# Performance work log

Hardware: AMD Instinct MI355X
Metric: run time of the kernel (lower is better)

Reference implementation:

```python
import jax, jax.numpy as jnp
import numpy as np

D = 4096  # in_features == out_features (required: LayerNorm(in_features) applied to out-dim output)
B, S = 4, 4096
LN_EPS = 1e-5


def setup_inputs() -> dict:
    key = jax.random.key(0)
    ks = jax.random.split(key, 5)
    return {
        "x": jax.random.normal(ks[0], (B, S, D), dtype=jnp.float32),
        "weight": jax.random.normal(ks[1], (D, D), dtype=jnp.float32),  # [out, in]
        "bias": jax.random.normal(ks[2], (D,), dtype=jnp.float32),
        "g": jax.random.normal(ks[3], (D,), dtype=jnp.float32),   # input scale [in]
        "h": jax.random.normal(ks[4], (D,), dtype=jnp.float32),   # output scale [out]
        "ln_gamma": jnp.ones((D,), dtype=jnp.float32),
        "ln_beta": jnp.zeros((D,), dtype=jnp.float32),
    }


def reference(x, weight, bias, g, h, ln_gamma, ln_beta):
    sign_w = jnp.sign(weight)                      # binarized weight [out, in]
    xg = x * g                                     # per-input-channel scale
    y = jnp.einsum("bsi,oi->bso", xg, sign_w) + bias
    y = y * h                                      # per-output-channel scale
    mu = jnp.mean(y, axis=-1, keepdims=True)
    var = jnp.mean(jnp.square(y - mu), axis=-1, keepdims=True)
    out = (y - mu) * jax.lax.rsqrt(var + LN_EPS) * ln_gamma + ln_beta
    return out
```

## Files before the change

### kernel.cpp

```cpp
#include <hip/hip_runtime.h>
#include <hip/hip_bf16.h>
#include <stdint.h>

typedef __bf16 bf16x8 __attribute__((ext_vector_type(8)));
typedef float f32x4 __attribute__((ext_vector_type(4)));

#define GLDS16(gp, lp) __builtin_amdgcn_global_load_lds( \
    (const __attribute__((address_space(1))) unsigned int*)(gp), \
    (__attribute__((address_space(3))) unsigned int*)(lp), 16, 0, 0)

#define BARRIER() asm volatile("s_barrier" ::: "memory")
#define VMCNT(n)  asm volatile("s_waitcnt vmcnt(" #n ")" ::: "memory")


__global__ __launch_bounds__(256) void prep_xg(
    const float* __restrict__ x, const float* __restrict__ g,
    __bf16* __restrict__ out, long total, int K)
{
    long i = ((long)blockIdx.x * blockDim.x + threadIdx.x) * 8;
    const long stride = (long)gridDim.x * blockDim.x * 8;
    for (; i < total; i += stride) {
        const int k = (int)(i & (long)(K - 1));
        f32x4 x0 = *(const f32x4*)(x + i);
        f32x4 x1 = *(const f32x4*)(x + i + 4);
        f32x4 g0 = *(const f32x4*)(g + k);
        f32x4 g1 = *(const f32x4*)(g + k + 4);
        bf16x8 o;
        #pragma unroll
        for (int j = 0; j < 4; ++j) o[j]     = (__bf16)(x0[j] * g0[j]);
        #pragma unroll
        for (int j = 0; j < 4; ++j) o[4 + j] = (__bf16)(x1[j] * g1[j]);
        *(bf16x8*)(out + i) = o;
    }
}

__global__ __launch_bounds__(256) void prep_sign(
    const float* __restrict__ w, __bf16* __restrict__ out, long total)
{
    long i = ((long)blockIdx.x * blockDim.x + threadIdx.x) * 8;
    const long stride = (long)gridDim.x * blockDim.x * 8;
    for (; i < total; i += stride) {
        f32x4 w0 = *(const f32x4*)(w + i);
        f32x4 w1 = *(const f32x4*)(w + i + 4);
        bf16x8 o;
        #pragma unroll
        for (int j = 0; j < 4; ++j)
            o[j]     = (__bf16)((w0[j] > 0.f) ? 1.f : ((w0[j] < 0.f) ? -1.f : 0.f));
        #pragma unroll
        for (int j = 0; j < 4; ++j)
            o[4 + j] = (__bf16)((w1[j] > 0.f) ? 1.f : ((w1[j] < 0.f) ? -1.f : 0.f));
        *(bf16x8*)(out + i) = o;
    }
}


__global__ __launch_bounds__(512, 2) void gemm_8p(
    const __bf16* __restrict__ A, const __bf16* __restrict__ B,
    const float* __restrict__ bias, const float* __restrict__ h,
    float* __restrict__ y, int M, int N, int K)
{
    extern __shared__ __bf16 sm[];

    const int xcd = blockIdx.x & 7;
    const int l = blockIdx.x >> 3;
    const int bn = xcd * 2 + (l >> 6);
    const int bm = l & 63;

    const int t = threadIdx.x;
    const int lane = t & 63;
    const int w = t >> 6;
    const int wm = w >> 2;
    const int wn = w & 3;
    const int sl = lane >> 4;
    const int fr = lane & 15;

    const int ra8 = (wm * 16 + fr) * 8;
    const int rb8 = (wn * 16 + fr) * 8;
    const int stA = w * 2048 + lane * 8;
    const int stB = 16384 + stA;

    const __bf16* gA = A + (long)(bm * 256 + lane) * K + w * 8;
    const __bf16* gB = B + (long)(bn * 256 + lane) * K + w * 8;

    const int NT = K / 64;
    const long K64 = (long)K * 64;
    const long K128 = (long)K * 128;

#define STG_A(c, T, half) do { \
    GLDS16(gA + (long)(half) * K128 + (long)(T) * 64,             &sm[(c) * 32768 + stA + (half) * 1024]); \
    GLDS16(gA + (long)(half) * K128 + K64 + (long)(T) * 64,       &sm[(c) * 32768 + stA + (half) * 1024 + 512]); \
} while (0)
#define STG_B(c, T, half) do { \
    GLDS16(gB + (long)(half) * K128 + (long)(T) * 64,             &sm[(c) * 32768 + stB + (half) * 1024]); \
    GLDS16(gB + (long)(half) * K128 + K64 + (long)(T) * 64,       &sm[(c) * 32768 + stB + (half) * 1024 + 512]); \
} while (0)

#define RD_A(dst, cb, m, kk)  dst = *(bf16x8*)&sm[(cb) + ((kk) * 4 + sl) * 2048 + (m) * 256 + ra8]
#define RD_B(dst, cb, n, kk)  dst = *(bf16x8*)&sm[(cb) + 16384 + ((kk) * 4 + sl) * 2048 + (n) * 512 + rb8]
#define MF(d, a, b) d = __builtin_amdgcn_mfma_f32_16x16x32_bf16(a, b, d, 0, 0, 0)

    f32x4 acc[8][4] = {};
    bf16x8 aF[4][2], aH[4][2], b0F[2][2], b1F[2][2];

    STG_A(0, 0, 0); STG_B(0, 0, 0); STG_B(0, 0, 1); STG_A(0, 0, 1);
    STG_A(1, 1, 0); STG_B(1, 1, 0); STG_B(1, 1, 1);
    VMCNT(6);
    BARRIER();

    for (int i = 0; i < NT / 2; ++i) {
        const int t1 = 2 * i + 1;
        const int nx0 = 2 * i + 2;
        const int nx1 = 2 * i + 3;
        const bool more = (nx0 < NT);

        #pragma unroll
        for (int kk = 0; kk < 2; ++kk) {
            #pragma unroll
            for (int m = 0; m < 4; ++m) RD_A(aF[m][kk], 0, m, kk);
            #pragma unroll
            for (int n = 0; n < 2; ++n) RD_B(b0F[n][kk], 0, n, kk);
        }
        STG_A(1, t1, 1);
        BARRIER();
        __builtin_amdgcn_s_setprio(1);
        #pragma unroll
        for (int kk = 0; kk < 2; ++kk)
            #pragma unroll
            for (int m = 0; m < 4; ++m)
                #pragma unroll
                for (int n = 0; n < 2; ++n) MF(acc[m][n], aF[m][kk], b0F[n][kk]);
        __builtin_amdgcn_s_setprio(0);
        BARRIER();

        #pragma unroll
        for (int kk = 0; kk < 2; ++kk)
            #pragma unroll
            for (int n = 0; n < 2; ++n) RD_B(b1F[n][kk], 0, n + 2, kk);
        if (more) STG_A(0, nx0, 0);
        BARRIER();
        __builtin_amdgcn_s_setprio(1);
        #pragma unroll
        for (int kk = 0; kk < 2; ++kk)
            #pragma unroll
            for (int m = 0; m < 4; ++m)
                #pragma unroll
                for (int n = 0; n < 2; ++n) MF(acc[m][n + 2], aF[m][kk], b1F[n][kk]);
        __builtin_amdgcn_s_setprio(0);
        BARRIER();

        #pragma unroll
        for (int kk = 0; kk < 2; ++kk)
            #pragma unroll
            for (int m = 0; m < 4; ++m) RD_A(aH[m][kk], 0, m + 4, kk);
        if (more) STG_B(0, nx0, 0);
        BARRIER();
        __builtin_amdgcn_s_setprio(1);
        #pragma unroll
        for (int kk = 0; kk < 2; ++kk)
            #pragma unroll
            for (int m = 0; m < 4; ++m)
                #pragma unroll
                for (int n = 0; n < 2; ++n) MF(acc[m + 4][n], aH[m][kk], b0F[n][kk]);
        __builtin_amdgcn_s_setprio(0);
        BARRIER();

        if (more) { STG_B(0, nx0, 1); VMCNT(6); } else { VMCNT(0); }
        BARRIER();
        __builtin_amdgcn_s_setprio(1);
        #pragma unroll
        for (int kk = 0; kk < 2; ++kk)
            #pragma unroll
            for (int m = 0; m < 4; ++m)
                #pragma unroll
                for (int n = 0; n < 2; ++n) MF(acc[m + 4][n + 2], aH[m][kk], b1F[n][kk]);
        __builtin_amdgcn_s_setprio(0);
        BARRIER();

        #pragma unroll
        for (int kk = 0; kk < 2; ++kk) {
            #pragma unroll
            for (int m = 0; m < 4; ++m) RD_A(aF[m][kk], 32768, m, kk);
            #pragma unroll
            for (int n = 0; n < 2; ++n) RD_B(b0F[n][kk], 32768, n, kk);
        }
        if (more) STG_A(0, nx0, 1);
        BARRIER();
        __builtin_amdgcn_s_setprio(1);
        #pragma unroll
        for (int kk = 0; kk < 2; ++kk)
            #pragma unroll
            for (int m = 0; m < 4; ++m)
                #pragma unroll
                for (int n = 0; n < 2; ++n) MF(acc[m][n], aF[m][kk], b0F[n][kk]);
        __builtin_amdgcn_s_setprio(0);
        BARRIER();

        #pragma unroll
        for (int kk = 0; kk < 2; ++kk)
            #pragma unroll
            for (int n = 0; n < 2; ++n) RD_B(b1F[n][kk], 32768, n + 2, kk);
        if (more) STG_A(1, nx1, 0);
        BARRIER();
        __builtin_amdgcn_s_setprio(1);
        #pragma unroll
        for (int kk = 0; kk < 2; ++kk)
            #pragma unroll
            for (int m = 0; m < 4; ++m)
                #pragma unroll
                for (int n = 0; n < 2; ++n) MF(acc[m][n + 2], aF[m][kk], b1F[n][kk]);
        __builtin_amdgcn_s_setprio(0);
        BARRIER();

        #pragma unroll
        for (int kk = 0; kk < 2; ++kk)
            #pragma unroll
            for (int m = 0; m < 4; ++m) RD_A(aH[m][kk], 32768, m + 4, kk);
        if (more) STG_B(1, nx1, 0);
        BARRIER();
        __builtin_amdgcn_s_setprio(1);
        #pragma unroll
        for (int kk = 0; kk < 2; ++kk)
            #pragma unroll
            for (int m = 0; m < 4; ++m)
                #pragma unroll
                for (int n = 0; n < 2; ++n) MF(acc[m + 4][n], aH[m][kk], b0F[n][kk]);
        __builtin_amdgcn_s_setprio(0);
        BARRIER();

        if (more) { STG_B(1, nx1, 1); VMCNT(6); } else { VMCNT(0); }
        BARRIER();
        __builtin_amdgcn_s_setprio(1);
        #pragma unroll
        for (int kk = 0; kk < 2; ++kk)
            #pragma unroll
            for (int m = 0; m < 4; ++m)
                #pragma unroll
                for (int n = 0; n < 2; ++n) MF(acc[m + 4][n + 2], aH[m][kk], b1F[n][kk]);
        __builtin_amdgcn_s_setprio(0);
        BARRIER();
    }

    const int cr = (lane >> 4) * 4;
    const int cc = lane & 15;
    #pragma unroll
    for (int n = 0; n < 4; ++n) {
        const int col = bn * 256 + n * 64 + wn * 16 + cc;
        const float bc = bias[col];
        const float hc = h[col];
        #pragma unroll
        for (int m = 0; m < 8; ++m) {
            const long rowb = (long)bm * 256 + m * 32 + wm * 16 + cr;
            #pragma unroll
            for (int j = 0; j < 4; ++j)
                y[(rowb + j) * N + col] = (acc[m][n][j] + bc) * hc;
        }
    }
#undef STG_A
#undef STG_B
#undef RD_A
#undef RD_B
#undef MF
}


__global__ __launch_bounds__(256) void ln_inplace(
    float* __restrict__ y, const float* __restrict__ gamma,
    const float* __restrict__ beta, int N)
{
    const long row = blockIdx.x;
    float* p = y + row * (long)N;
    const int t = threadIdx.x;

    f32x4 v[4];
    float sum = 0.f, sq = 0.f;
    #pragma unroll
    for (int i = 0; i < 4; ++i) {
        v[i] = *(const f32x4*)(p + i * 1024 + t * 4);
        #pragma unroll
        for (int j = 0; j < 4; ++j) { sum += v[i][j]; sq += v[i][j] * v[i][j]; }
    }
    #pragma unroll
    for (int off = 32; off > 0; off >>= 1) {
        sum += __shfl_down(sum, off);
        sq  += __shfl_down(sq, off);
    }
    __shared__ float s1[4], s2[4];
    const int lane = t & 63, wave = t >> 6;
    if (lane == 0) { s1[wave] = sum; s2[wave] = sq; }
    __syncthreads();
    const float tot = s1[0] + s1[1] + s1[2] + s1[3];
    const float tsq = s2[0] + s2[1] + s2[2] + s2[3];
    const float mean = tot / (float)N;
    const float var = tsq / (float)N - mean * mean;
    const float rstd = rsqrtf(var + 1e-5f);

    #pragma unroll
    for (int i = 0; i < 4; ++i) {
        f32x4 ga = *(const f32x4*)(gamma + i * 1024 + t * 4);
        f32x4 be = *(const f32x4*)(beta + i * 1024 + t * 4);
        f32x4 o;
        #pragma unroll
        for (int j = 0; j < 4; ++j) o[j] = (v[i][j] - mean) * rstd * ga[j] + be[j];
        *(f32x4*)(p + i * 1024 + t * 4) = o;
    }
}


#define BMf 128
#define BNf 128
#define BKf 32
#define LDPf 40

__global__ __launch_bounds__(256) void binlin_gemm_fb(
    const float* __restrict__ x, const float* __restrict__ w,
    const float* __restrict__ bias, const float* __restrict__ g,
    const float* __restrict__ h, float* __restrict__ y,
    int M, int N, int K)
{
    __shared__ __bf16 As[BMf][LDPf];
    __shared__ __bf16 Bs[BNf][LDPf];
    const int nbn = N / BNf;
    const int bm = blockIdx.x / nbn;
    const int bn = blockIdx.x % nbn;
    const int t = threadIdx.x;
    const int lane = t & 63;
    const int wave = t >> 6;
    const int wm = wave >> 1, wn = wave & 1;
    const int row2 = t >> 2, kq = (t & 3) * 8;
    const long xbase = (long)bm * BMf * K;
    const long wbase = (long)bn * BNf * K;
    f32x4 acc[4][4] = {};
    const int fr = lane & 15;
    const int ko = (lane >> 4) * 8;
    for (int k0 = 0; k0 < K; k0 += BKf) {
        f32x4 ga = *(const f32x4*)(g + k0 + kq);
        f32x4 gb = *(const f32x4*)(g + k0 + kq + 4);
        #pragma unroll
        for (int p = 0; p < 2; ++p) {
            const int r = p * 64 + row2;
            const float* xp = x + xbase + (long)r * K + k0 + kq;
            f32x4 x0 = *(const f32x4*)xp;
            f32x4 x1 = *(const f32x4*)(xp + 4);
            bf16x8 av;
            #pragma unroll
            for (int i = 0; i < 4; ++i) av[i]     = (__bf16)(x0[i] * ga[i]);
            #pragma unroll
            for (int i = 0; i < 4; ++i) av[4 + i] = (__bf16)(x1[i] * gb[i]);
            *(bf16x8*)&As[r][kq] = av;
            const float* wp = w + wbase + (long)r * K + k0 + kq;
            f32x4 w0 = *(const f32x4*)wp;
            f32x4 w1 = *(const f32x4*)(wp + 4);
            bf16x8 bv;
            #pragma unroll
            for (int i = 0; i < 4; ++i)
                bv[i]     = (__bf16)((w0[i] > 0.f) ? 1.f : ((w0[i] < 0.f) ? -1.f : 0.f));
            #pragma unroll
            for (int i = 0; i < 4; ++i)
                bv[4 + i] = (__bf16)((w1[i] > 0.f) ? 1.f : ((w1[i] < 0.f) ? -1.f : 0.f));
            *(bf16x8*)&Bs[r][kq] = bv;
        }
        __syncthreads();
        bf16x8 af[4], bfr[4];
        #pragma unroll
        for (int m = 0; m < 4; ++m) af[m]  = *(bf16x8*)&As[wm * 64 + m * 16 + fr][ko];
        #pragma unroll
        for (int n = 0; n < 4; ++n) bfr[n] = *(bf16x8*)&Bs[wn * 64 + n * 16 + fr][ko];
        #pragma unroll
        for (int m = 0; m < 4; ++m)
            #pragma unroll
            for (int n = 0; n < 4; ++n)
                acc[m][n] = __builtin_amdgcn_mfma_f32_16x16x32_bf16(af[m], bfr[n], acc[m][n], 0, 0, 0);
        __syncthreads();
    }
    const int cr = (lane >> 4) * 4;
    const int cc = lane & 15;
    #pragma unroll
    for (int n = 0; n < 4; ++n) {
        const int col = bn * BNf + wn * 64 + n * 16 + cc;
        const float bc = bias[col];
        const float hc = h[col];
        #pragma unroll
        for (int m = 0; m < 4; ++m) {
            const long rowb = (long)bm * BMf + wm * 64 + m * 16 + cr;
            #pragma unroll
            for (int j = 0; j < 4; ++j)
                y[(rowb + j) * N + col] = (acc[m][n][j] + bc) * hc;
        }
    }
}

extern "C" void kernel_launch(void* const* d_in, const int* in_sizes, int n_in,
                              void* d_out, int out_size, void* d_ws, size_t ws_size,
                              hipStream_t stream)
{
    (void)n_in; (void)out_size;
    const float* x     = (const float*)d_in[0];
    const float* w     = (const float*)d_in[1];
    const float* bias  = (const float*)d_in[2];
    const float* g     = (const float*)d_in[3];
    const float* h     = (const float*)d_in[4];
    const float* gamma = (const float*)d_in[5];
    const float* beta  = (const float*)d_in[6];
    float* out = (float*)d_out;

    const int D = in_sizes[2];
    const long M = (long)in_sizes[0] / D;

    const size_t needA = (size_t)M * D * sizeof(__bf16);
    const size_t needB = (size_t)D * D * sizeof(__bf16);

    if (ws_size >= needA + needB && (M % 256) == 0 && (D % 256) == 0 &&
        (D % 128) == 0 && ((M / 256) * (D / 256)) % 8 == 0) {
        __bf16* xg   = (__bf16*)d_ws;
        __bf16* wsgn = (__bf16*)((char*)d_ws + needA);
        prep_xg  <<<dim3(2048), dim3(256), 0, stream>>>(x, g, xg, M * (long)D, D);
        prep_sign<<<dim3(2048), dim3(256), 0, stream>>>(w, wsgn, (long)D * D);
        hipFuncSetAttribute((const void*)gemm_8p,
                            hipFuncAttributeMaxDynamicSharedMemorySize, 131072);
        dim3 grid((unsigned)((M / 256) * (D / 256)));
        gemm_8p<<<grid, dim3(512), 131072, stream>>>(xg, wsgn, bias, h, out, (int)M, D, D);
    } else {
        dim3 grid((unsigned)((M / BMf) * (D / BNf)));
        binlin_gemm_fb<<<grid, dim3(256), 0, stream>>>(x, w, bias, g, h, out, (int)M, D, D);
    }
    ln_inplace<<<dim3((unsigned)M), dim3(256), 0, stream>>>(out, gamma, beta, D);
}
```

Measured before the change: 792.0 us.

## Store GEMM output as bf16 in workspace and fuse two-row LayerNorm

The GEMM epilogue now writes the scaled output as bf16 with nontemporal stores into a workspace buffer. A new LayerNorm kernel handles two rows per block, reads that bf16 buffer and writes fp32 output, replacing the fp32 write and read-back of the intermediate. The block-to-tile mapping is also changed so consecutive blocks alternate between N tiles. Rounding the pre-LayerNorm values to bf16 adds error, and the single-pass variance formula (E[x²]−μ²) can lose precision.

```diff
diff --git a/kernel.cpp b/kernel.cpp
--- a/kernel.cpp
+++ b/kernel.cpp
@@ -54,17 +54,18 @@
 }
 
 
+template<bool BF16OUT>
 __global__ __launch_bounds__(512, 2) void gemm_8p(
     const __bf16* __restrict__ A, const __bf16* __restrict__ B,
     const float* __restrict__ bias, const float* __restrict__ h,
-    float* __restrict__ y, int M, int N, int K)
+    __bf16* __restrict__ yb, float* __restrict__ yf, int M, int N, int K)
 {
     extern __shared__ __bf16 sm[];
 
     const int xcd = blockIdx.x & 7;
     const int l = blockIdx.x >> 3;
-    const int bn = xcd * 2 + (l >> 6);
-    const int bm = l & 63;
+    const int bn = xcd * 2 + (l & 1);
+    const int bm = l >> 1;
 
     const int t = threadIdx.x;
     const int lane = t & 63;
@@ -251,8 +252,17 @@
         for (int m = 0; m < 8; ++m) {
             const long rowb = (long)bm * 256 + m * 32 + wm * 16 + cr;
             #pragma unroll
-            for (int j = 0; j < 4; ++j)
-                y[(rowb + j) * N + col] = (acc[m][n][j] + bc) * hc;
+            for (int j = 0; j < 4; ++j) {
+                const float v = (acc[m][n][j] + bc) * hc;
+                if (BF16OUT) {
+                    union { __bf16 b; unsigned short u; } cv;
+                    cv.b = (__bf16)v;
+                    __builtin_nontemporal_store(cv.u,
+                        (unsigned short*)yb + (rowb + j) * (long)N + col);
+                } else {
+                    __builtin_nontemporal_store(v, yf + (rowb + j) * (long)N + col);
+                }
+            }
         }
     }
 #undef STG_A
@@ -260,6 +270,64 @@
 #undef RD_A
 #undef RD_B
 #undef MF
+}
+
+
+__global__ __launch_bounds__(256) void ln_ws(
+    const __bf16* __restrict__ ybuf, float* __restrict__ out,
+    const float* __restrict__ gamma, const float* __restrict__ beta)
+{
+    const long r0 = (long)blockIdx.x * 2;
+    const int t = threadIdx.x;
+    const int lane = t & 63, wave = t >> 6;
+
+    bf16x8 a0 = *(const bf16x8*)(ybuf + r0 * 4096 + t * 16);
+    bf16x8 a1 = *(const bf16x8*)(ybuf + r0 * 4096 + t * 16 + 8);
+    bf16x8 b0 = *(const bf16x8*)(ybuf + (r0 + 1) * 4096 + t * 16);
+    bf16x8 b1 = *(const bf16x8*)(ybuf + (r0 + 1) * 4096 + t * 16 + 8);
+
+    float v0[16], v1[16];
+    float s0 = 0.f, q0 = 0.f, s1 = 0.f, q1 = 0.f;
+    #pragma unroll
+    for (int j = 0; j < 8; ++j) {
+        v0[j] = (float)a0[j]; v0[8 + j] = (float)a1[j];
+        v1[j] = (float)b0[j]; v1[8 + j] = (float)b1[j];
+    }
+    #pragma unroll
+    for (int j = 0; j < 16; ++j) {
+        s0 += v0[j]; q0 += v0[j] * v0[j];
+        s1 += v1[j]; q1 += v1[j] * v1[j];
+    }
+    #pragma unroll
+    for (int off = 32; off > 0; off >>= 1) {
+        s0 += __shfl_down(s0, off); q0 += __shfl_down(q0, off);
+        s1 += __shfl_down(s1, off); q1 += __shfl_down(q1, off);
+    }
+    __shared__ float red[4][4];
+    if (lane == 0) { red[wave][0] = s0; red[wave][1] = q0; red[wave][2] = s1; red[wave][3] = q1; }
+    __syncthreads();
+    const float ts0 = red[0][0] + red[1][0] + red[2][0] + red[3][0];
+    const float tq0 = red[0][1] + red[1][1] + red[2][1] + red[3][1];
+    const float ts1 = red[0][2] + red[1][2] + red[2][2] + red[3][2];
+    const float tq1 = red[0][3] + red[1][3] + red[2][3] + red[3][3];
+    const float mu0 = ts0 * (1.0f / 4096.0f);
+    const float mu1 = ts1 * (1.0f / 4096.0f);
+    const float rs0 = rsqrtf(tq0 * (1.0f / 4096.0f) - mu0 * mu0 + 1e-5f);
+    const float rs1 = rsqrtf(tq1 * (1.0f / 4096.0f) - mu1 * mu1 + 1e-5f);
+
+    #pragma unroll
+    for (int c = 0; c < 4; ++c) {
+        f32x4 gv = *(const f32x4*)(gamma + t * 16 + c * 4);
+        f32x4 bv = *(const f32x4*)(beta + t * 16 + c * 4);
+        f32x4 o0, o1;
+        #pragma unroll
+        for (int j = 0; j < 4; ++j) {
+            o0[j] = (v0[c * 4 + j] - mu0) * rs0 * gv[j] + bv[j];
+            o1[j] = (v1[c * 4 + j] - mu1) * rs1 * gv[j] + bv[j];
+        }
+        *(f32x4*)(out + r0 * 4096 + t * 16 + c * 4) = o0;
+        *(f32x4*)(out + (r0 + 1) * 4096 + t * 16 + c * 4) = o1;
+    }
 }
 
 
@@ -408,20 +476,34 @@
 
     const size_t needA = (size_t)M * D * sizeof(__bf16);
     const size_t needB = (size_t)D * D * sizeof(__bf16);
-
-    if (ws_size >= needA + needB && (M % 256) == 0 && (D % 256) == 0 &&
-        (D % 128) == 0 && ((M / 256) * (D / 256)) % 8 == 0) {
+    const size_t needY = (size_t)M * D * sizeof(__bf16);
+
+    const bool okShape = (D == 4096 && (M % 512) == 0);
+
+    if (okShape && ws_size >= needA + needB) {
         __bf16* xg   = (__bf16*)d_ws;
         __bf16* wsgn = (__bf16*)((char*)d_ws + needA);
         prep_xg  <<<dim3(2048), dim3(256), 0, stream>>>(x, g, xg, M * (long)D, D);
         prep_sign<<<dim3(2048), dim3(256), 0, stream>>>(w, wsgn, (long)D * D);
-        hipFuncSetAttribute((const void*)gemm_8p,
-                            hipFuncAttributeMaxDynamicSharedMemorySize, 131072);
         dim3 grid((unsigned)((M / 256) * (D / 256)));
-        gemm_8p<<<grid, dim3(512), 131072, stream>>>(xg, wsgn, bias, h, out, (int)M, D, D);
+
+        if (ws_size >= needA + needB + needY) {
+            __bf16* ybf = (__bf16*)((char*)d_ws + needA + needB);
+            hipFuncSetAttribute((const void*)gemm_8p<true>,
+                                hipFuncAttributeMaxDynamicSharedMemorySize, 131072);
+            gemm_8p<true><<<grid, dim3(512), 131072, stream>>>(
+                xg, wsgn, bias, h, ybf, nullptr, (int)M, D, D);
+            ln_ws<<<dim3((unsigned)(M / 2)), dim3(256), 0, stream>>>(ybf, out, gamma, beta);
+        } else {
+            hipFuncSetAttribute((const void*)gemm_8p<false>,
+                                hipFuncAttributeMaxDynamicSharedMemorySize, 131072);
+            gemm_8p<false><<<grid, dim3(512), 131072, stream>>>(
+                xg, wsgn, bias, h, nullptr, out, (int)M, D, D);
+            ln_inplace<<<dim3((unsigned)M), dim3(256), 0, stream>>>(out, gamma, beta, D);
+        }
     } else {
         dim3 grid((unsigned)((M / BMf) * (D / BNf)));
         binlin_gemm_fb<<<grid, dim3(256), 0, stream>>>(x, w, bias, g, h, out, (int)M, D, D);
-    }
-    ln_inplace<<<dim3((unsigned)M), dim3(256), 0, stream>>>(out, gamma, beta, D);
-}
+        ln_inplace<<<dim3((unsigned)M), dim3(256), 0, stream>>>(out, gamma, beta, D);
+    }
+}
```

Result: no change. 778.2 us (-1.7%).
